# Kernel tuning notes

Hardware: AMD Instinct MI355X
Metric: run time of the kernel (lower is better)

## Reference

```python
import jax, jax.numpy as jnp
import numpy as np

B, S, E = 4, 2048, 512
H, D = 8, 64  # n_head, attn_dim


def setup_inputs() -> dict:
    key = jax.random.key(0)
    ks = jax.random.split(key, 12)
    scale = 0.02
    return {
        "input_q": jax.random.normal(ks[0], (B, S, E), dtype=jnp.float32),
        "input_k": jax.random.normal(ks[1], (B, S, E), dtype=jnp.float32),
        "input_v": jax.random.normal(ks[2], (B, S, E), dtype=jnp.float32),
        "mask": jax.random.randint(ks[3], (B, S, S), 0, 2, dtype=jnp.int32),
        "wq": jax.random.normal(ks[4], (E, H * D), dtype=jnp.float32) * scale,
        "bq": jnp.zeros((H * D,), dtype=jnp.float32),
        "wk": jax.random.normal(ks[5], (E, H * D), dtype=jnp.float32) * scale,
        "bk": jnp.zeros((H * D,), dtype=jnp.float32),
        "wv": jax.random.normal(ks[6], (E, H * D), dtype=jnp.float32) * scale,
        "bv": jnp.zeros((H * D,), dtype=jnp.float32),
        "wo": jax.random.normal(ks[7], (H * D, E), dtype=jnp.float32) * scale,
        "bo": jnp.zeros((E,), dtype=jnp.float32),
    }


def reference(input_q, input_k, input_v, mask, wq, bq, wk, bk, wv, bv, wo, bo):
    b, lq, _ = input_q.shape
    lk = input_k.shape[1]
    # projections -> [b, len, H, D] -> [b, H, len, D]
    q = (input_q @ wq + bq).reshape(b, lq, H, D).transpose(0, 2, 1, 3)
    k = (input_k @ wk + bk).reshape(b, lk, H, D).transpose(0, 2, 1, 3)
    v = (input_v @ wv + bv).reshape(b, lk, H, D).transpose(0, 2, 1, 3)
    # raw scores [b, H, lq, lk]
    score = jnp.einsum("bhqd,bhkd->bhqk", q, k)
    # NOTE: original masks with -1e9 BEFORE dividing by sqrt(attn_dim)
    score = jnp.where(mask[:, None, :, :] == 0, jnp.float32(-1e9), score)
    attn = jax.nn.softmax(score / jnp.sqrt(jnp.float32(D)), axis=-1)
    out = jnp.einsum("bhqk,bhkd->bqhd", attn, v).reshape(b, lq, H * D)
    return out @ wo + bo
```

## Files before the change

### kernel.cpp

```cpp
#include <hip/hip_runtime.h>
#include <hip/hip_bf16.h>
#include <stdint.h>

#define Bc 4
#define Sc 2048
#define Ec 512
#define Hc 8
#define Dc 64
#define HDc 512

typedef __attribute__((ext_vector_type(8))) short bf16x8;
typedef __attribute__((ext_vector_type(4))) float f32x4;
typedef unsigned int u32;

__device__ __forceinline__ unsigned short f2bf(float x) {
    union { float f; unsigned u; } v; v.f = x;
    unsigned r = v.u + 0x7FFFu + ((v.u >> 16) & 1u);
    return (unsigned short)(r >> 16);
}

__device__ __forceinline__ unsigned pkbf2(float a, float b) {
    float2 f; f.x = a; f.y = b;
    __hip_bfloat162 h = __float22bfloat162_rn(f);
    union { __hip_bfloat162 h2; unsigned u; } u; u.h2 = h;
    return u.u;
}

__device__ __forceinline__ uint4 pack8(float4 a, float4 b) {
    uint4 v;
    v.x = pkbf2(a.x, a.y); v.y = pkbf2(a.z, a.w);
    v.z = pkbf2(b.x, b.y); v.w = pkbf2(b.z, b.w);
    return v;
}

__device__ __forceinline__ void gload_lds(const void* g, void* l) {
    __builtin_amdgcn_global_load_lds(
        (const __attribute__((address_space(1))) u32*)g,
        (__attribute__((address_space(3))) u32*)l,
        16, 0, 0);
}

__global__ __launch_bounds__(256) void pack_mask(const int* __restrict__ mask,
                                                 unsigned long long* __restrict__ bits) {
    const int lane = threadIdx.x & 63;
    int wave = (blockIdx.x * blockDim.x + threadIdx.x) >> 6;
    const int nwaves = (gridDim.x * blockDim.x) >> 6;
    const int nwords = (Bc * Sc * Sc) / 64;
    for (int w = wave; w < nwords; w += nwaves) {
        int m = mask[(size_t)w * 64 + lane];
        unsigned long long b = __ballot(m != 0);
        if (lane == 0) bits[w] = b;
    }
}

__global__ __launch_bounds__(256) void transpose_w(
    const float* __restrict__ W0, const float* __restrict__ W1,
    const float* __restrict__ W2, const float* __restrict__ W3,
    unsigned short* __restrict__ Wt)
{
    const int z = blockIdx.z;
    const float* W = z == 0 ? W0 : (z == 1 ? W1 : (z == 2 ? W2 : W3));
    unsigned short* O = Wt + (size_t)z * Ec * HDc;
    __shared__ float t[64][65];
    const int k0 = blockIdx.x * 64, n0 = blockIdx.y * 64;
#pragma unroll
    for (int i = 0; i < 16; i++) {
        int idx = threadIdx.x + 256 * i;
        int kr = idx >> 6, nc = idx & 63;
        t[nc][kr] = W[(size_t)(k0 + kr) * HDc + n0 + nc];
    }
    __syncthreads();
#pragma unroll
    for (int i = 0; i < 16; i++) {
        int idx = threadIdx.x + 256 * i;
        int nr = idx >> 6, kc = idx & 63;
        O[(size_t)(n0 + nr) * Ec + k0 + kc] = f2bf(t[nr][kc]);
    }
}

__global__ __launch_bounds__(256) void proj_gemm(
    const float* __restrict__ Xq, const float* __restrict__ Xk, const float* __restrict__ Xv,
    const unsigned short* __restrict__ Wt,
    const float* __restrict__ bq, const float* __restrict__ bk, const float* __restrict__ bv,
    unsigned short* __restrict__ Oq, unsigned short* __restrict__ Ok,
    unsigned short* __restrict__ Vt)
{
    const int z = blockIdx.z;
    const float* X = z == 0 ? Xq : (z == 1 ? Xk : Xv);
    const unsigned short* Bt = Wt + (size_t)z * Ec * HDc;
    const float* bias = z == 0 ? bq : (z == 1 ? bk : bv);

    const int n0 = blockIdx.x * 128;
    const int m0 = blockIdx.y * 128;
    const int tid = threadIdx.x, lane = tid & 63, w = tid >> 6;
    const int c = lane & 15, quad = lane >> 4;
    const int wm = w & 1, wn = w >> 1;

    __shared__ unsigned short As[128 * 64];
    __shared__ unsigned short Bs[128 * 64];

    f32x4 acc[4][4];
#pragma unroll
    for (int i = 0; i < 4; i++)
#pragma unroll
        for (int j = 0; j < 4; j++) acc[i][j] = (f32x4){0.f, 0.f, 0.f, 0.f};

    for (int k0 = 0; k0 < Ec; k0 += 64) {
        __syncthreads();
#pragma unroll
        for (int jj = 0; jj < 4; jj++) {
            int rb = w * 32 + jj * 8;
            int row = rb + (lane >> 3);
            int dg = (lane & 7) ^ (row & 7);
            gload_lds(Bt + (size_t)(n0 + row) * Ec + k0 + dg * 8, &Bs[rb * 64]);
        }
#pragma unroll
        for (int s = 0; s < 4; s++) {
            int idx = tid + 256 * s;
            int row = idx >> 3, kp = idx & 7;
            int dg = kp ^ (row & 7);
            const float* src = X + (size_t)(m0 + row) * Ec + k0 + dg * 8;
            float4 fa = *(const float4*)src;
            float4 fb = *(const float4*)(src + 4);
            *(uint4*)&As[row * 64 + kp * 8] = pack8(fa, fb);
        }
        __syncthreads();
#pragma unroll
        for (int ks = 0; ks < 2; ks++) {
            int kg = ks * 4 + quad;
            bf16x8 af[4], bfr[4];
#pragma unroll
            for (int mt = 0; mt < 4; mt++) {
                int row = wm * 64 + mt * 16 + c;
                af[mt] = *(const bf16x8*)&As[row * 64 + ((kg ^ (row & 7)) * 8)];
            }
#pragma unroll
            for (int nt = 0; nt < 4; nt++) {
                int row = wn * 64 + nt * 16 + c;
                bfr[nt] = *(const bf16x8*)&Bs[row * 64 + ((kg ^ (row & 7)) * 8)];
            }
            if (z < 2) {
#pragma unroll
                for (int mt = 0; mt < 4; mt++)
#pragma unroll
                    for (int nt = 0; nt < 4; nt++)
                        acc[mt][nt] = __builtin_amdgcn_mfma_f32_16x16x32_bf16(af[mt], bfr[nt], acc[mt][nt], 0, 0, 0);
            } else {
#pragma unroll
                for (int mt = 0; mt < 4; mt++)
#pragma unroll
                    for (int nt = 0; nt < 4; nt++)
                        acc[mt][nt] = __builtin_amdgcn_mfma_f32_16x16x32_bf16(bfr[nt], af[mt], acc[mt][nt], 0, 0, 0);
            }
        }
    }

    if (z < 2) {
        unsigned short* O = z == 0 ? Oq : Ok;
#pragma unroll
        for (int mt = 0; mt < 4; mt++)
#pragma unroll
            for (int r = 0; r < 4; r++) {
                int gm = m0 + wm * 64 + mt * 16 + quad * 4 + r;
#pragma unroll
                for (int nt = 0; nt < 4; nt++) {
                    int gn = n0 + wn * 64 + nt * 16 + c;
                    O[(size_t)gm * HDc + gn] = f2bf(acc[mt][nt][r] + bias[gn]);
                }
            }
    } else {
#pragma unroll
        for (int mt = 0; mt < 4; mt++) {
            int gm = m0 + wm * 64 + mt * 16 + c;
            int bb = gm >> 11, sPos = gm & (Sc - 1);
#pragma unroll
            for (int nt = 0; nt < 4; nt++)
#pragma unroll
                for (int r = 0; r < 4; r++) {
                    int ng = n0 + wn * 64 + nt * 16 + quad * 4 + r;
                    int hh = ng >> 6, d = ng & 63;
                    Vt[((size_t)(bb * Hc + hh) * Dc + d) * Sc + sPos] = f2bf(acc[mt][nt][r] + bias[ng]);
                }
        }
    }
}

__global__ __launch_bounds__(256, 4) void attn_kernel(
    const unsigned short* __restrict__ Qb, const unsigned short* __restrict__ Kb,
    const unsigned short* __restrict__ Vt, const unsigned long long* __restrict__ Mb,
    unsigned short* __restrict__ Ob)
{
    const int qt = blockIdx.x;
    const int h  = blockIdx.y;
    const int b  = blockIdx.z;
    const int q0 = qt * 64;
    const int tid = threadIdx.x, lane = tid & 63, w = tid >> 6;
    const int c = lane & 15, quad = lane >> 4;

    __shared__ unsigned short Ks[2][64 * 64];
    __shared__ unsigned short Vs[2][64 * 64];
    __shared__ unsigned short Pt[64 * 64];

    const int qg = q0 + w * 16 + c;
    const size_t qoff = ((size_t)b * Sc + qg) * HDc + h * Dc;

    bf16x8 qf[2];
    qf[0] = *(const bf16x8*)(Qb + qoff + quad * 8);
    qf[1] = *(const bf16x8*)(Qb + qoff + 32 + quad * 8);

    const unsigned long long* mr = Mb + ((size_t)b * Sc + qg) * (Sc / 64);
    const size_t kbase = ((size_t)b * Sc) * HDc + h * Dc;
    const size_t vbase = ((size_t)(b * Hc + h)) * Dc * Sc;

    f32x4 o[4];
#pragma unroll
    for (int i = 0; i < 4; i++) o[i] = (f32x4){0.f, 0.f, 0.f, 0.f};
    float lsum = 0.f;

    unsigned short* ptrow = &Pt[(w * 16 + c) * 64];
    const int sw = (c & 7) << 1;

    auto stage = [&](int kt, int buf) {
#pragma unroll
        for (int j = 0; j < 2; j++) {
            int rb = w * 16 + j * 8;
            int row = rb + (lane >> 3);
            int dg = (lane & 7) ^ (row & 7);
            gload_lds(Kb + kbase + (size_t)(kt * 64 + row) * HDc + dg * 8, &Ks[buf][rb * 64]);
            gload_lds(Vt + vbase + (size_t)row * Sc + kt * 64 + dg * 8, &Vs[buf][rb * 64]);
        }
    };

    stage(0, 0);
    for (int kt = 0; kt < Sc / 64; kt++) {
        const int cur = kt & 1;
        unsigned long long mw = mr[kt];
        __syncthreads();
        if (kt + 1 < Sc / 64) stage(kt + 1, cur ^ 1);

        f32x4 s[4];
#pragma unroll
        for (int nt = 0; nt < 4; nt++) s[nt] = (f32x4){0.f, 0.f, 0.f, 0.f};
#pragma unroll
        for (int ks = 0; ks < 2; ks++) {
            int kg = ks * 4 + quad;
#pragma unroll
            for (int nt = 0; nt < 4; nt++) {
                int t = nt * 16 + c;
                bf16x8 a = *(const bf16x8*)&Ks[cur][t * 64 + ((kg ^ (t & 7)) * 8)];
                s[nt] = __builtin_amdgcn_mfma_f32_16x16x32_bf16(a, qf[ks], s[nt], 0, 0, 0);
            }
        }

        u32 nlo = ~(u32)(mw >> (quad * 4));
        u32 nhi = ~(u32)(mw >> (quad * 4 + 32));
#pragma unroll
        for (int nt = 0; nt < 4; nt++) {
            u32 msrc = (nt < 2) ? nlo : nhi;
            float p[4];
#pragma unroll
            for (int r = 0; r < 4; r++) {
                const int sh = (nt & 1) * 16 + r;
                int tneg = ((int)(msrc << (31 - sh))) >> 31;
                float bias = __int_as_float(tneg & 0xC4800000);
                p[r] = exp2f(fmaf(s[nt][r], 0.18033688f, bias));
                lsum += p[r];
            }
            uint2 pk; pk.x = pkbf2(p[0], p[1]); pk.y = pkbf2(p[2], p[3]);
            int u = nt * 4 + quad;
            *(uint2*)(ptrow + ((u ^ sw) << 2)) = pk;
        }

#pragma unroll
        for (int ks = 0; ks < 2; ks++) {
            int u1 = ks * 8 + quad * 2;
            bf16x8 pf = *(const bf16x8*)(ptrow + ((u1 ^ sw) << 2));
            int kg = ks * 4 + quad;
#pragma unroll
            for (int nt = 0; nt < 4; nt++) {
                int d = nt * 16 + c;
                bf16x8 a = *(const bf16x8*)&Vs[cur][d * 64 + ((kg ^ (d & 7)) * 8)];
                o[nt] = __builtin_amdgcn_mfma_f32_16x16x32_bf16(a, pf, o[nt], 0, 0, 0);
            }
        }
    }

    lsum += __shfl_xor(lsum, 16, 64);
    lsum += __shfl_xor(lsum, 32, 64);
    float inv = 1.0f / lsum;

#pragma unroll
    for (int nt = 0; nt < 4; nt++) {
        uint2 pk;
        pk.x = pkbf2(o[nt][0] * inv, o[nt][1] * inv);
        pk.y = pkbf2(o[nt][2] * inv, o[nt][3] * inv);
        *(uint2*)(Ob + qoff + nt * 16 + quad * 4) = pk;
    }
}

__global__ __launch_bounds__(256) void out_gemm(
    const unsigned short* __restrict__ Ab, const unsigned short* __restrict__ Bt,
    const float* __restrict__ bias, float* __restrict__ Out)
{
    const int n0 = blockIdx.x * 128;
    const int m0 = blockIdx.y * 64;
    const int tid = threadIdx.x, lane = tid & 63, w = tid >> 6;
    const int c = lane & 15, quad = lane >> 4;
    const int wm = w & 1, wn = w >> 1;

    __shared__ unsigned short As[64 * 64];
    __shared__ unsigned short Bs[128 * 64];

    f32x4 acc[2][4];
#pragma unroll
    for (int i = 0; i < 2; i++)
#pragma unroll
        for (int j = 0; j < 4; j++) acc[i][j] = (f32x4){0.f, 0.f, 0.f, 0.f};

    for (int k0 = 0; k0 < HDc; k0 += 64) {
        __syncthreads();
#pragma unroll
        for (int jj = 0; jj < 4; jj++) {
            int rb = w * 32 + jj * 8;
            int row = rb + (lane >> 3);
            int dg = (lane & 7) ^ (row & 7);
            gload_lds(Bt + (size_t)(n0 + row) * Ec + k0 + dg * 8, &Bs[rb * 64]);
        }
#pragma unroll
        for (int jj = 0; jj < 2; jj++) {
            int rb = w * 16 + jj * 8;
            int row = rb + (lane >> 3);
            int dg = (lane & 7) ^ (row & 7);
            gload_lds(Ab + (size_t)(m0 + row) * HDc + k0 + dg * 8, &As[rb * 64]);
        }
        __syncthreads();
#pragma unroll
        for (int ks = 0; ks < 2; ks++) {
            int kg = ks * 4 + quad;
            bf16x8 af[2], bfr[4];
#pragma unroll
            for (int mt = 0; mt < 2; mt++) {
                int row = wm * 32 + mt * 16 + c;
                af[mt] = *(const bf16x8*)&As[row * 64 + ((kg ^ (row & 7)) * 8)];
            }
#pragma unroll
            for (int nt = 0; nt < 4; nt++) {
                int row = wn * 64 + nt * 16 + c;
                bfr[nt] = *(const bf16x8*)&Bs[row * 64 + ((kg ^ (row & 7)) * 8)];
            }
#pragma unroll
            for (int mt = 0; mt < 2; mt++)
#pragma unroll
                for (int nt = 0; nt < 4; nt++)
                    acc[mt][nt] = __builtin_amdgcn_mfma_f32_16x16x32_bf16(af[mt], bfr[nt], acc[mt][nt], 0, 0, 0);
        }
    }
#pragma unroll
    for (int mt = 0; mt < 2; mt++)
#pragma unroll
        for (int r = 0; r < 4; r++) {
            int gm = m0 + wm * 32 + mt * 16 + quad * 4 + r;
#pragma unroll
            for (int nt = 0; nt < 4; nt++) {
                int gn = n0 + wn * 64 + nt * 16 + c;
                Out[(size_t)gm * Ec + gn] = acc[mt][nt][r] + bias[gn];
            }
        }
}

extern "C" void kernel_launch(void* const* d_in, const int* in_sizes, int n_in,
                              void* d_out, int out_size, void* d_ws, size_t ws_size,
                              hipStream_t stream)
{
    const float* xq = (const float*)d_in[0];
    const float* xk = (const float*)d_in[1];
    const float* xv = (const float*)d_in[2];
    const int* mask = (const int*)d_in[3];
    const float* wq = (const float*)d_in[4];
    const float* bq = (const float*)d_in[5];
    const float* wk = (const float*)d_in[6];
    const float* bk = (const float*)d_in[7];
    const float* wv = (const float*)d_in[8];
    const float* bv = (const float*)d_in[9];
    const float* wo = (const float*)d_in[10];
    const float* bo = (const float*)d_in[11];
    float* out = (float*)d_out;

    char* ws = (char*)d_ws;
    unsigned short* qb = (unsigned short*)(ws + (size_t)0 * 1024 * 1024);
    unsigned short* kb = (unsigned short*)(ws + (size_t)8 * 1024 * 1024);
    unsigned short* vt = (unsigned short*)(ws + (size_t)16 * 1024 * 1024);
    unsigned short* ab = (unsigned short*)(ws + (size_t)24 * 1024 * 1024);
    unsigned long long* mb = (unsigned long long*)(ws + (size_t)32 * 1024 * 1024);
    unsigned short* wt = (unsigned short*)(ws + (size_t)48 * 1024 * 1024);

    hipLaunchKernelGGL(pack_mask, dim3(2048), dim3(256), 0, stream, mask, mb);
    hipLaunchKernelGGL(transpose_w, dim3(8, 8, 4), dim3(256), 0, stream,
                       wq, wk, wv, wo, wt);

    const size_t WSZ = (size_t)Ec * HDc;
    hipLaunchKernelGGL(proj_gemm, dim3(4, 64, 3), dim3(256), 0, stream,
                       xq, xk, xv, wt, bq, bk, bv, qb, kb, vt);

    hipLaunchKernelGGL(attn_kernel, dim3(32, 8, 4), dim3(256), 0, stream,
                       qb, kb, vt, mb, ab);

    hipLaunchKernelGGL(out_gemm, dim3(4, 128), dim3(256), 0, stream,
                       ab, wt + 3 * WSZ, bo, out);
}
```

Measured before the change: 301.7 us.

## Keep softmax probabilities in registers via f16 MFMA and fold scale into Q

The attention kernel drops the LDS round trip for the probability tile. Exponentials are packed to fp16 in registers and fed straight into 16x16x16 f16 MFMAs against an fp16 V tile, whose layout now matches the score accumulator layout. The row sum comes from an extra MFMA against a ones vector instead of shuffles, and masked entries are zeroed with a bitmask rather than a large negative bias. The 1/sqrt(D) scale is folded into the Q projection epilogue, and the mask-pack and weight-transpose kernels are merged into one launch. The trade-offs are fp16 range and precision for V and P, and no max subtraction, which relies on scores staying small.

```diff
diff --git a/kernel.cpp b/kernel.cpp
--- a/kernel.cpp
+++ b/kernel.cpp
@@ -1,5 +1,6 @@
 #include <hip/hip_runtime.h>
 #include <hip/hip_bf16.h>
+#include <hip/hip_fp16.h>
 #include <stdint.h>
 
 #define Bc 4
@@ -10,6 +11,7 @@
 #define HDc 512
 
 typedef __attribute__((ext_vector_type(8))) short bf16x8;
+typedef __attribute__((ext_vector_type(4))) _Float16 f16x4;
 typedef __attribute__((ext_vector_type(4))) float f32x4;
 typedef unsigned int u32;
 
@@ -26,6 +28,16 @@
     return u.u;
 }
 
+__device__ __forceinline__ unsigned short f2h(float x) {
+    return __half_as_ushort(__float2half_rn(x));
+}
+
+__device__ __forceinline__ unsigned pkh2(float a, float b) {
+    union { __half2 h2; unsigned u; } u;
+    u.h2 = __floats2half2_rn(a, b);
+    return u.u;
+}
+
 __device__ __forceinline__ uint4 pack8(float4 a, float4 b) {
     uint4 v;
     v.x = pkbf2(a.x, a.y); v.y = pkbf2(a.z, a.w);
@@ -40,41 +52,42 @@
         16, 0, 0);
 }
 
-__global__ __launch_bounds__(256) void pack_mask(const int* __restrict__ mask,
-                                                 unsigned long long* __restrict__ bits) {
-    const int lane = threadIdx.x & 63;
-    int wave = (blockIdx.x * blockDim.x + threadIdx.x) >> 6;
-    const int nwaves = (gridDim.x * blockDim.x) >> 6;
-    const int nwords = (Bc * Sc * Sc) / 64;
-    for (int w = wave; w < nwords; w += nwaves) {
-        int m = mask[(size_t)w * 64 + lane];
-        unsigned long long b = __ballot(m != 0);
-        if (lane == 0) bits[w] = b;
-    }
-}
-
-__global__ __launch_bounds__(256) void transpose_w(
+__global__ __launch_bounds__(256) void prep(
+    const int* __restrict__ mask, unsigned long long* __restrict__ bits,
     const float* __restrict__ W0, const float* __restrict__ W1,
     const float* __restrict__ W2, const float* __restrict__ W3,
     unsigned short* __restrict__ Wt)
 {
-    const int z = blockIdx.z;
-    const float* W = z == 0 ? W0 : (z == 1 ? W1 : (z == 2 ? W2 : W3));
-    unsigned short* O = Wt + (size_t)z * Ec * HDc;
+    const int blk = blockIdx.x;
     __shared__ float t[64][65];
-    const int k0 = blockIdx.x * 64, n0 = blockIdx.y * 64;
-#pragma unroll
-    for (int i = 0; i < 16; i++) {
-        int idx = threadIdx.x + 256 * i;
-        int kr = idx >> 6, nc = idx & 63;
-        t[nc][kr] = W[(size_t)(k0 + kr) * HDc + n0 + nc];
-    }
-    __syncthreads();
-#pragma unroll
-    for (int i = 0; i < 16; i++) {
-        int idx = threadIdx.x + 256 * i;
-        int nr = idx >> 6, kc = idx & 63;
-        O[(size_t)(n0 + nr) * Ec + k0 + kc] = f2bf(t[nr][kc]);
+    if (blk < 256) {
+        const int z = blk >> 6;
+        const float* W = z == 0 ? W0 : (z == 1 ? W1 : (z == 2 ? W2 : W3));
+        unsigned short* O = Wt + (size_t)z * Ec * HDc;
+        const int k0 = ((blk >> 3) & 7) * 64, n0 = (blk & 7) * 64;
+#pragma unroll
+        for (int i = 0; i < 16; i++) {
+            int idx = threadIdx.x + 256 * i;
+            int kr = idx >> 6, nc = idx & 63;
+            t[nc][kr] = W[(size_t)(k0 + kr) * HDc + n0 + nc];
+        }
+        __syncthreads();
+#pragma unroll
+        for (int i = 0; i < 16; i++) {
+            int idx = threadIdx.x + 256 * i;
+            int nr = idx >> 6, kc = idx & 63;
+            O[(size_t)(n0 + nr) * Ec + k0 + kc] = f2bf(t[nr][kc]);
+        }
+    } else {
+        const int lane = threadIdx.x & 63;
+        int wave = ((blk - 256) * 256 + (int)threadIdx.x) >> 6;
+        const int nwaves = (2048 * 256) >> 6;
+        const int nwords = (Bc * Sc * Sc) / 64;
+        for (int w = wave; w < nwords; w += nwaves) {
+            int m = mask[(size_t)w * 64 + lane];
+            unsigned long long b = __ballot(m != 0);
+            if (lane == 0) bits[w] = b;
+        }
     }
 }
 
@@ -157,6 +170,7 @@
 
     if (z < 2) {
         unsigned short* O = z == 0 ? Oq : Ok;
+        const float qs = z == 0 ? 0.125f : 1.0f;
 #pragma unroll
         for (int mt = 0; mt < 4; mt++)
 #pragma unroll
@@ -165,7 +179,7 @@
 #pragma unroll
                 for (int nt = 0; nt < 4; nt++) {
                     int gn = n0 + wn * 64 + nt * 16 + c;
-                    O[(size_t)gm * HDc + gn] = f2bf(acc[mt][nt][r] + bias[gn]);
+                    O[(size_t)gm * HDc + gn] = f2bf((acc[mt][nt][r] + bias[gn]) * qs);
                 }
             }
     } else {
@@ -179,7 +193,7 @@
                 for (int r = 0; r < 4; r++) {
                     int ng = n0 + wn * 64 + nt * 16 + quad * 4 + r;
                     int hh = ng >> 6, d = ng & 63;
-                    Vt[((size_t)(bb * Hc + hh) * Dc + d) * Sc + sPos] = f2bf(acc[mt][nt][r] + bias[ng]);
+                    Vt[((size_t)(bb * Hc + hh) * Dc + d) * Sc + sPos] = f2h(acc[mt][nt][r] + bias[ng]);
                 }
         }
     }
@@ -199,7 +213,6 @@
 
     __shared__ unsigned short Ks[2][64 * 64];
     __shared__ unsigned short Vs[2][64 * 64];
-    __shared__ unsigned short Pt[64 * 64];
 
     const int qg = q0 + w * 16 + c;
     const size_t qoff = ((size_t)b * Sc + qg) * HDc + h * Dc;
@@ -212,13 +225,12 @@
     const size_t kbase = ((size_t)b * Sc) * HDc + h * Dc;
     const size_t vbase = ((size_t)(b * Hc + h)) * Dc * Sc;
 
-    f32x4 o[4];
+    f32x4 o[4], osum;
 #pragma unroll
     for (int i = 0; i < 4; i++) o[i] = (f32x4){0.f, 0.f, 0.f, 0.f};
-    float lsum = 0.f;
-
-    unsigned short* ptrow = &Pt[(w * 16 + c) * 64];
-    const int sw = (c & 7) << 1;
+    osum = (f32x4){0.f, 0.f, 0.f, 0.f};
+
+    const f16x4 ones = {(_Float16)1.0f, (_Float16)1.0f, (_Float16)1.0f, (_Float16)1.0f};
 
     auto stage = [&](int kt, int buf) {
 #pragma unroll
@@ -252,42 +264,40 @@
             }
         }
 
-        u32 nlo = ~(u32)(mw >> (quad * 4));
-        u32 nhi = ~(u32)(mw >> (quad * 4 + 32));
+        u32 mlo = (u32)(mw) >> (quad * 4);
+        u32 mhi = (u32)(mw >> 32) >> (quad * 4);
+        f16x4 pb[4];
 #pragma unroll
         for (int nt = 0; nt < 4; nt++) {
-            u32 msrc = (nt < 2) ? nlo : nhi;
+            u32 msrc = (nt < 2) ? mlo : mhi;
             float p[4];
 #pragma unroll
             for (int r = 0; r < 4; r++) {
                 const int sh = (nt & 1) * 16 + r;
-                int tneg = ((int)(msrc << (31 - sh))) >> 31;
-                float bias = __int_as_float(tneg & 0xC4800000);
-                p[r] = exp2f(fmaf(s[nt][r], 0.18033688f, bias));
-                lsum += p[r];
-            }
-            uint2 pk; pk.x = pkbf2(p[0], p[1]); pk.y = pkbf2(p[2], p[3]);
-            int u = nt * 4 + quad;
-            *(uint2*)(ptrow + ((u ^ sw) << 2)) = pk;
-        }
-
-#pragma unroll
-        for (int ks = 0; ks < 2; ks++) {
-            int u1 = ks * 8 + quad * 2;
-            bf16x8 pf = *(const bf16x8*)(ptrow + ((u1 ^ sw) << 2));
-            int kg = ks * 4 + quad;
-#pragma unroll
-            for (int nt = 0; nt < 4; nt++) {
-                int d = nt * 16 + c;
-                bf16x8 a = *(const bf16x8*)&Vs[cur][d * 64 + ((kg ^ (d & 7)) * 8)];
-                o[nt] = __builtin_amdgcn_mfma_f32_16x16x32_bf16(a, pf, o[nt], 0, 0, 0);
-            }
-        }
-    }
-
-    lsum += __shfl_xor(lsum, 16, 64);
-    lsum += __shfl_xor(lsum, 32, 64);
-    float inv = 1.0f / lsum;
+                int keep = ((int)(msrc << (31 - sh))) >> 31;
+                float e = __expf(s[nt][r]);
+                p[r] = __int_as_float(__float_as_int(e) & keep);
+            }
+            union { unsigned u[2]; f16x4 v; } pk;
+            pk.u[0] = pkh2(p[0], p[1]);
+            pk.u[1] = pkh2(p[2], p[3]);
+            pb[nt] = pk.v;
+        }
+
+#pragma unroll
+        for (int ntb = 0; ntb < 4; ntb++) {
+#pragma unroll
+            for (int dt = 0; dt < 4; dt++) {
+                int d = dt * 16 + c;
+                const f16x4 a = *(const f16x4*)&Vs[cur][d * 64 +
+                    (((ntb * 2 + (quad >> 1)) ^ (d & 7)) * 8) + ((quad & 1) * 4)];
+                o[dt] = __builtin_amdgcn_mfma_f32_16x16x16f16(a, pb[ntb], o[dt], 0, 0, 0);
+            }
+            osum = __builtin_amdgcn_mfma_f32_16x16x16f16(ones, pb[ntb], osum, 0, 0, 0);
+        }
+    }
+
+    const float inv = 1.0f / osum[0];
 
 #pragma unroll
     for (int nt = 0; nt < 4; nt++) {
@@ -394,9 +404,8 @@
     unsigned long long* mb = (unsigned long long*)(ws + (size_t)32 * 1024 * 1024);
     unsigned short* wt = (unsigned short*)(ws + (size_t)48 * 1024 * 1024);
 
-    hipLaunchKernelGGL(pack_mask, dim3(2048), dim3(256), 0, stream, mask, mb);
-    hipLaunchKernelGGL(transpose_w, dim3(8, 8, 4), dim3(256), 0, stream,
-                       wq, wk, wv, wo, wt);
+    hipLaunchKernelGGL(prep, dim3(2304), dim3(256), 0, stream,
+                       mask, mb, wq, wk, wv, wo, wt);
 
     const size_t WSZ = (size_t)Ec * HDc;
     hipLaunchKernelGGL(proj_gemm, dim3(4, 64, 3), dim3(256), 0, stream,
```

Result: faster. 287.7 us (-4.6%).
